# Kernel optimization log

Hardware: AMD Instinct MI355X
Metric: run time of the kernel (lower is better)

The kernel has to match this reference:

```python
import jax, jax.numpy as jnp
import numpy as np

DIM = 1024
HEADS = 16
HEAD_DIM = DIM // HEADS
FF = 4096
B, S = 2, 2048
EPS = 1e-6
NEG = float(jnp.finfo(jnp.float32).min)


def rmsnorm(x, w):
    return x * jax.lax.rsqrt(jnp.mean(x * x, axis=-1, keepdims=True) + EPS) * w


def setup_inputs() -> dict:
    key = jax.random.key(0)
    ks = jax.random.split(key, 12)
    s = 1.0 / np.sqrt(DIM)
    return {
        "x": jax.random.normal(ks[0], (B, S, DIM), jnp.float32),
        "src_key_padding_mask": jax.random.randint(ks[1], (B, S), 0, 2).astype(bool),
        "rel_pos_bias": jax.random.normal(ks[2], (1, HEADS, S, S), jnp.float32),
        "Wq": jax.random.normal(ks[3], (DIM, DIM), jnp.float32) * s,
        "Wk": jax.random.normal(ks[4], (DIM, DIM), jnp.float32) * s,
        "Wv": jax.random.normal(ks[5], (DIM, DIM), jnp.float32) * s,
        "Wo": jax.random.normal(ks[6], (DIM, DIM), jnp.float32) * s,
        "W1": jax.random.normal(ks[7], (DIM, FF), jnp.float32) * s,
        "b1": jnp.zeros((FF,), jnp.float32),
        "W2": jax.random.normal(ks[8], (FF, DIM), jnp.float32) * (1.0 / np.sqrt(FF)),
        "b2": jnp.zeros((DIM,), jnp.float32),
        "g1": jnp.ones((DIM,), jnp.float32),
        "g2": jnp.ones((DIM,), jnp.float32),
    }


def reference(x, src_key_padding_mask, rel_pos_bias, Wq, Wk, Wv, Wo, W1, b1, W2, b2, g1, g2):
    # pre-norm self-attention
    h = rmsnorm(x, g1)  # [B,S,D]
    q = (h @ Wq).reshape(B, S, HEADS, HEAD_DIM).transpose(0, 2, 1, 3)
    k = (h @ Wk).reshape(B, S, HEADS, HEAD_DIM).transpose(0, 2, 1, 3)
    v = (h @ Wv).reshape(B, S, HEADS, HEAD_DIM).transpose(0, 2, 1, 3)
    scale = HEAD_DIM ** -0.5
    scores = jnp.einsum('bhqd,bhkd->bhqk', q, k) * scale + rel_pos_bias
    scores = jnp.where(src_key_padding_mask[:, None, None, :], NEG, scores)
    attn = jax.nn.softmax(scores, axis=-1)
    out = jnp.einsum('bhqk,bhkd->bhqd', attn, v)
    out = out.transpose(0, 2, 1, 3).reshape(B, S, DIM) @ Wo
    x = x + out
    # GELU FFN (exact erf gelu, matching torch F.gelu default)
    h2 = rmsnorm(x, g2)
    h2 = jax.nn.gelu(h2 @ W1 + b1, approximate=False) @ W2 + b2
    return x + h2
```

## Files before the change

kernel.cpp:

```cpp
#include <hip/hip_runtime.h>
#include <math.h>

typedef __attribute__((ext_vector_type(8))) short   short8;
typedef __attribute__((ext_vector_type(4))) short   short4v;
typedef __attribute__((ext_vector_type(8))) __bf16  bf16x8;
typedef __attribute__((ext_vector_type(4))) float   f32x4;
typedef __attribute__((ext_vector_type(16))) float  f32x16;
typedef unsigned short u16;

#define DIMD 1024
#define NHEAD 16
#define HD 64
#define FFD 4096
#define BB 2
#define SSEQ 2048
#define NSPLIT 2
#define KVSPAN (SSEQ / NSPLIT)
#define NROWS (BB * NHEAD * SSEQ)
#define NEGF -3.4028235e38f

__device__ __forceinline__ u16 f2bf(float f){
  unsigned u = __float_as_uint(f);
  u += 0x7FFFu + ((u >> 16) & 1u);
  return (u16)(u >> 16);
}
__device__ __forceinline__ float bf2f(u16 v){
  return __uint_as_float(((unsigned)v) << 16);
}
__device__ __forceinline__ void gload16(const u16* g, u16* l){
  __builtin_amdgcn_global_load_lds((const __attribute__((address_space(1))) void*)g,
                                   (__attribute__((address_space(3))) void*)l, 16, 0, 0);
}

__global__ void normalize_mask(const unsigned char* __restrict__ m, unsigned char* __restrict__ outm){
  __shared__ int any;
  if (threadIdx.x == 0) any = 0;
  __syncthreads();
  int bad = 0;
  for (int i = threadIdx.x; i < BB * SSEQ; i += 1024)
    if ((i & 3) && m[i]) bad = 1;
  if (bad) atomicOr(&any, 1);
  __syncthreads();
  bool is_i32 = (any == 0);
  if (is_i32){
    const int* mi = (const int*)m;
    for (int k = threadIdx.x; k < BB * SSEQ; k += 1024)
      outm[k] = (unsigned char)(mi[k] != 0);
  } else {
    for (int k = threadIdx.x; k < BB * SSEQ; k += 1024)
      outm[k] = m[k] ? 1 : 0;
  }
}

__global__ void transpose_to_bf16(const float* __restrict__ W, u16* __restrict__ Wt, int K, int N){
  __shared__ float tile[32][33];
  int n0 = blockIdx.x * 32, k0 = blockIdx.y * 32;
  int tx = threadIdx.x, ty = threadIdx.y;
  #pragma unroll
  for (int i = 0; i < 32; i += 8)
    tile[ty + i][tx] = W[(size_t)(k0 + ty + i) * N + n0 + tx];
  __syncthreads();
  #pragma unroll
  for (int i = 0; i < 32; i += 8)
    Wt[(size_t)(n0 + ty + i) * K + k0 + tx] = f2bf(tile[tx][ty + i]);
}

__global__ void vtrans(const u16* __restrict__ qkv, u16* __restrict__ vt){
  __shared__ u16 tile[32][33];
  int s0 = blockIdx.x * 32, d0 = blockIdx.y * 32;
  int bh = blockIdx.z;
  int b = bh >> 4, h = bh & 15;
  int tx = threadIdx.x, ty = threadIdx.y;
  const u16* src = qkv + (size_t)(b * SSEQ) * 3072 + 2048 + h * HD + d0;
  #pragma unroll
  for (int i = 0; i < 32; i += 8)
    tile[ty + i][tx] = src[(size_t)(s0 + ty + i) * 3072 + tx];
  __syncthreads();
  u16* dst = vt + ((size_t)bh * HD + d0) * SSEQ + s0;
  #pragma unroll
  for (int i = 0; i < 32; i += 8)
    dst[(size_t)(ty + i) * SSEQ + tx] = tile[tx][ty + i];
}

__global__ __launch_bounds__(256) void rmsnorm_k(const float* __restrict__ x, const float* __restrict__ g,
                                                 u16* __restrict__ out, int D){
  int row = blockIdx.x;
  const float* xr = x + (size_t)row * D;
  float ss = 0.f;
  for (int i = threadIdx.x * 4; i < D; i += 1024){
    float4 v = *(const float4*)&xr[i];
    ss += v.x*v.x + v.y*v.y + v.z*v.z + v.w*v.w;
  }
  #pragma unroll
  for (int o = 32; o > 0; o >>= 1) ss += __shfl_down(ss, o);
  __shared__ float red[4];
  if ((threadIdx.x & 63) == 0) red[threadIdx.x >> 6] = ss;
  __syncthreads();
  float tot = red[0] + red[1] + red[2] + red[3];
  float rs = rsqrtf(tot / (float)D + 1e-6f);
  for (int i = threadIdx.x * 4; i < D; i += 1024){
    float4 v  = *(const float4*)&xr[i];
    float4 gv = *(const float4*)&g[i];
    ushort4 o4;
    o4.x = f2bf(v.x * rs * gv.x);
    o4.y = f2bf(v.y * rs * gv.y);
    o4.z = f2bf(v.z * rs * gv.z);
    o4.w = f2bf(v.w * rs * gv.w);
    *(ushort4*)&out[(size_t)row * D + i] = o4;
  }
}

__device__ __forceinline__ void xcd_swz(int& bx, int& by){
  int gx = gridDim.x, nwg = gx * gridDim.y;
  int flat = by * gx + bx;
  int q = nwg >> 3;
  flat = (flat & 7) * q + (flat >> 3);
  bx = flat % gx;
  by = flat / gx;
}

template<int EPI>
__global__ __launch_bounds__(512, 2) void gemm8p(const u16* __restrict__ A, const u16* __restrict__ Bt,
                                                 u16* __restrict__ outb, const float* __restrict__ bias,
                                                 int M, int N, int K){
  extern __shared__ u16 lds[];
  const int tid = threadIdx.x;
  const int lane = tid & 63, lr = lane >> 4, lc = lane & 15;
  const int wid = tid >> 6, wr = wid >> 2, wc = wid & 3;
  int bx = blockIdx.x, by = blockIdx.y;
  xcd_swz(bx, by);
  const int m0 = by * 256, n0 = bx * 256;
  const int NT = K >> 5;
  const int slot8 = ((lr ^ (lc & 3)) << 3);

  f32x4 acc[8][4];
  #pragma unroll
  for (int i = 0; i < 8; i++)
    #pragma unroll
    for (int j = 0; j < 4; j++) acc[i][j] = (f32x4){0.f,0.f,0.f,0.f};

  const int srow = tid >> 2;
  const int scg  = (tid & 3) ^ (srow & 3);

  auto stage = [&](int t, int buf, int rsel){
    int row = ((rsel & 1) << 7) + srow;
    const u16* src = ((rsel < 2) ? A + (size_t)(m0 + row) * K
                                 : Bt + (size_t)(n0 + row) * K) + t * 32 + scg * 8;
    u16* dst = lds + buf * 16384 + ((rsel & 2) << 12) + ((rsel & 1) << 12) + tid * 8;
    gload16(src, dst);
  };
  auto ldA = [&](int buf, int mi) -> bf16x8 {
    int ra = wr * 128 + mi * 16 + lc;
    return *(const bf16x8*)&lds[buf * 16384 + ra * 32 + slot8];
  };
  auto ldB = [&](int buf, int ni) -> bf16x8 {
    int rb = wc * 64 + ni * 16 + lc;
    return *(const bf16x8*)&lds[buf * 16384 + 8192 + rb * 32 + slot8];
  };

  #pragma unroll
  for (int rs = 0; rs < 4; rs++) stage(0, 0, rs);
  #pragma unroll
  for (int rs = 0; rs < 4; rs++) stage(1, 1, rs);
  asm volatile("s_waitcnt vmcnt(4)" ::: "memory");
  __builtin_amdgcn_s_barrier();

  int buf = 0;
  for (int t = 0; t < NT; t++){
    int sbuf = buf + 2; if (sbuf >= 3) sbuf -= 3;
    bool ds = (t + 2 < NT);
    bf16x8 a[4], b[4];
    #pragma unroll
    for (int mi = 0; mi < 4; mi++) a[mi] = ldA(buf, mi);
    #pragma unroll
    for (int ni = 0; ni < 4; ni++) b[ni] = ldB(buf, ni);
    if (ds){ stage(t + 2, sbuf, 0); stage(t + 2, sbuf, 1); }
    __builtin_amdgcn_s_barrier();
    __builtin_amdgcn_s_setprio(1);
    #pragma unroll
    for (int mi = 0; mi < 4; mi++)
      #pragma unroll
      for (int ni = 0; ni < 4; ni++)
        acc[mi][ni] = __builtin_amdgcn_mfma_f32_16x16x32_bf16(a[mi], b[ni], acc[mi][ni], 0, 0, 0);
    __builtin_amdgcn_s_setprio(0);
    __builtin_amdgcn_s_barrier();
    #pragma unroll
    for (int mi = 0; mi < 4; mi++) a[mi] = ldA(buf, mi + 4);
    if (ds){ stage(t + 2, sbuf, 2); stage(t + 2, sbuf, 3); }
    __builtin_amdgcn_s_barrier();
    __builtin_amdgcn_s_setprio(1);
    #pragma unroll
    for (int mi = 0; mi < 4; mi++)
      #pragma unroll
      for (int ni = 0; ni < 4; ni++)
        acc[mi + 4][ni] = __builtin_amdgcn_mfma_f32_16x16x32_bf16(a[mi], b[ni], acc[mi + 4][ni], 0, 0, 0);
    __builtin_amdgcn_s_setprio(0);
    if (t + 2 < NT)      { asm volatile("s_waitcnt vmcnt(4)" ::: "memory"); }
    else if (t + 1 < NT) { asm volatile("s_waitcnt vmcnt(0)" ::: "memory"); }
    __builtin_amdgcn_s_barrier();
    buf++; if (buf == 3) buf = 0;
  }

  #pragma unroll
  for (int mi = 0; mi < 8; mi++){
    #pragma unroll
    for (int ni = 0; ni < 4; ni++){
      int col = n0 + wc * 64 + ni * 16 + lc;
      #pragma unroll
      for (int r = 0; r < 4; r++){
        int row = m0 + wr * 128 + mi * 16 + lr * 4 + r;
        float v = acc[mi][ni][r];
        if (EPI == 2){
          v += bias[col];
          v = 0.5f * v * (1.f + erff(v * 0.70710678118654752f));
        }
        outb[(size_t)row * N + col] = f2bf(v);
      }
    }
  }
}

template<int EPI, int BN>
__global__ __launch_bounds__(256) void gemm_bt(const u16* __restrict__ A, const u16* __restrict__ Bt,
                                               u16* __restrict__ outb, float* __restrict__ outf,
                                               const float* __restrict__ bias, const float* __restrict__ resid,
                                               int M, int N, int K){
  constexpr int NI = BN / 32;
  __shared__ u16 As[128 * 64];
  __shared__ u16 Bs[BN * 64];
  const int tid = threadIdx.x;
  const int wid = tid >> 6, lane = tid & 63, lr = lane >> 4, lc = lane & 15;
  const int wr = wid >> 1, wc = wid & 1;
  int bx = blockIdx.x, by = blockIdx.y;
  xcd_swz(bx, by);
  const int m0 = by * 128, n0 = bx * BN;

  f32x4 acc[4][NI];
  #pragma unroll
  for (int i = 0; i < 4; i++)
    #pragma unroll
    for (int j = 0; j < NI; j++) acc[i][j] = (f32x4){0.f,0.f,0.f,0.f};

  for (int k0 = 0; k0 < K; k0 += 64){
    __syncthreads();
    #pragma unroll
    for (int j = 0; j < 4; j++){
      int c = tid + 256 * j;
      gload16(A + (size_t)(m0 + (c >> 3)) * K + k0 + (c & 7) * 8, As + c * 8);
    }
    #pragma unroll
    for (int j = 0; j < NI; j++){
      int c = tid + 256 * j;
      gload16(Bt + (size_t)(n0 + (c >> 3)) * K + k0 + (c & 7) * 8, Bs + c * 8);
    }
    __syncthreads();
    #pragma unroll
    for (int kk = 0; kk < 2; kk++){
      bf16x8 a[4], b[NI];
      #pragma unroll
      for (int mi = 0; mi < 4; mi++) a[mi] = *(const bf16x8*)&As[(wr*64 + mi*16 + lc)*64 + kk*32 + lr*8];
      #pragma unroll
      for (int ni = 0; ni < NI; ni++) b[ni] = *(const bf16x8*)&Bs[(wc*(BN/2) + ni*16 + lc)*64 + kk*32 + lr*8];
      #pragma unroll
      for (int mi = 0; mi < 4; mi++)
        #pragma unroll
        for (int ni = 0; ni < NI; ni++)
          acc[mi][ni] = __builtin_amdgcn_mfma_f32_16x16x32_bf16(a[mi], b[ni], acc[mi][ni], 0, 0, 0);
    }
  }

  #pragma unroll
  for (int mi = 0; mi < 4; mi++){
    #pragma unroll
    for (int ni = 0; ni < NI; ni++){
      #pragma unroll
      for (int r = 0; r < 4; r++){
        int row = m0 + wr*64 + mi*16 + lr*4 + r;
        int col = n0 + wc*(BN/2) + ni*16 + lc;
        float v = acc[mi][ni][r];
        size_t idx = (size_t)row * N + col;
        if (EPI == 0){
          outb[idx] = f2bf(v);
        } else if (EPI == 1){
          outf[idx] = v + resid[idx];
        } else if (EPI == 2){
          v += bias[col];
          v = 0.5f * v * (1.f + erff(v * 0.70710678118654752f));
          outb[idx] = f2bf(v);
        } else {
          outf[idx] = v + bias[col] + resid[idx];
        }
      }
    }
  }
}

__global__ __launch_bounds__(256) void attn_part(const u16* __restrict__ qkv, const u16* __restrict__ vt,
                                                 const float* __restrict__ bias,
                                                 const unsigned char* __restrict__ mask,
                                                 u16* __restrict__ Opart, float* __restrict__ mp, float* __restrict__ lp){
  __shared__ u16 Ks [64 * 64];
  __shared__ u16 Vts[64 * 64];
  __shared__ u16 Ps [4 * 32 * 72];

  const int tid = threadIdx.x;
  const int lane = tid & 63, hi = lane >> 5, lq = lane & 31;
  const int wq = tid >> 6;
  const int b  = blockIdx.x & 1;
  const int qb = blockIdx.x >> 1;
  const int h  = blockIdx.y;
  const int sp = blockIdx.z;
  const int qw = qb * 128 + wq * 32;
  const int kv_lo = sp * KVSPAN, kv_hi = kv_lo + KVSPAN;

  char* kls = (char*)Ks;
  char* vls = (char*)Vts;
  u16*  psw = Ps + wq * 32 * 72;

  bf16x8 qf[4];
  {
    const u16* qp = qkv + ((size_t)(b * SSEQ + qw + lq)) * 3072 + h * HD + hi * 8;
    #pragma unroll
    for (int dstep = 0; dstep < 4; dstep++) qf[dstep] = *(const bf16x8*)(qp + dstep * 16);
  }

  const u16* kbase = qkv + (size_t)b * SSEQ * 3072 + 1024 + h * HD;
  const u16* vbase = vt + (size_t)(b * NHEAD + h) * HD * SSEQ;
  const int c0 = tid, c1 = tid + 256;
  auto kaddr = [&](int kv0, int c){ return kbase + (size_t)(kv0 + (c >> 3)) * 3072 + (c & 7) * 8; };
  auto vaddr = [&](int kv0, int c){ return vbase + (size_t)(c >> 3) * SSEQ + kv0 + (c & 7) * 8; };
  auto sstore = [&](char* base, int c, short8 v){
    int byte = (c >> 3) * 128 + (c & 7) * 16;
    byte ^= ((c >> 3) & 7) << 4;
    *(short8*)(base + byte) = v;
  };

  const float* brow = bias + ((size_t)h * SSEQ + (qw + lq)) * SSEQ;
  const unsigned char* mbase = mask + b * SSEQ;

  short8 kr0 = *(const short8*)kaddr(kv_lo, c0);
  short8 kr1 = *(const short8*)kaddr(kv_lo, c1);
  short8 vr0 = *(const short8*)vaddr(kv_lo, c0);
  short8 vr1 = *(const short8*)vaddr(kv_lo, c1);

  float mrow = NEGF, lsum = 0.f;
  f32x16 oacc[2];
  #pragma unroll
  for (int g = 0; g < 2; g++)
    #pragma unroll
    for (int r = 0; r < 16; r++) oacc[g][r] = 0.f;

  for (int kv0 = kv_lo; kv0 < kv_hi; kv0 += 64){
    float4 bv[8]; unsigned mk[8];
    #pragma unroll
    for (int kg = 0; kg < 2; kg++)
      #pragma unroll
      for (int rq = 0; rq < 4; rq++){
        int base = kv0 + kg * 32 + 8 * rq + 4 * hi;
        bv[kg*4+rq] = *(const float4*)&brow[base];
        mk[kg*4+rq] = *(const unsigned*)&mbase[base];
      }

    __syncthreads();
    sstore(kls, c0, kr0); sstore(kls, c1, kr1);
    sstore(vls, c0, vr0); sstore(vls, c1, vr1);
    __syncthreads();

    {
      int nxt = (kv0 + 64 < kv_hi) ? kv0 + 64 : kv_lo;
      kr0 = *(const short8*)kaddr(nxt, c0);
      kr1 = *(const short8*)kaddr(nxt, c1);
      vr0 = *(const short8*)vaddr(nxt, c0);
      vr1 = *(const short8*)vaddr(nxt, c1);
    }

    f32x16 acc[2];
    #pragma unroll
    for (int g = 0; g < 2; g++)
      #pragma unroll
      for (int r = 0; r < 16; r++) acc[g][r] = 0.f;
    __builtin_amdgcn_s_setprio(1);
    #pragma unroll
    for (int kg = 0; kg < 2; kg++){
      int row = kg * 32 + lq;
      #pragma unroll
      for (int dstep = 0; dstep < 4; dstep++){
        int byte = row * 128 + dstep * 32 + hi * 16;
        byte ^= (row & 7) << 4;
        bf16x8 kf = *(const bf16x8*)(kls + byte);
        acc[kg] = __builtin_amdgcn_mfma_f32_32x32x16_bf16(kf, qf[dstep], acc[kg], 0, 0, 0);
      }
    }
    __builtin_amdgcn_s_setprio(0);

    float p[2][16];
    float tm = NEGF;
    #pragma unroll
    for (int kg = 0; kg < 2; kg++)
      #pragma unroll
      for (int r = 0; r < 16; r++){
        int g = kg * 4 + (r >> 2);
        bool m = ((mk[g] >> (8 * (r & 3))) & 0xffu) != 0;
        float v = acc[kg][r] * 0.125f + ((const float*)&bv[g])[r & 3];
        v = m ? NEGF : v;
        p[kg][r] = v;
        tm = fmaxf(tm, v);
      }
    tm = fmaxf(tm, __shfl_xor(tm, 32));

    if (__any(tm > mrow + 5.f)){
      float mnew = fmaxf(mrow, tm);
      float corr = __expf(mrow - mnew);
      lsum *= corr;
      mrow = mnew;
      #pragma unroll
      for (int r = 0; r < 16; r++){
        float cr = __shfl(corr, (r & 3) + 8 * (r >> 2) + 4 * hi);
        oacc[0][r] *= cr;
        oacc[1][r] *= cr;
      }
    }

    float psum = 0.f;
    #pragma unroll
    for (int kg = 0; kg < 2; kg++)
      #pragma unroll
      for (int r = 0; r < 16; r++){
        float sv = p[kg][r];
        float e = (sv < -1e30f) ? 0.f : __expf(sv - mrow);
        p[kg][r] = e;
        psum += e;
      }
    psum += __shfl_xor(psum, 32);
    lsum += psum;

    #pragma unroll
    for (int kg = 0; kg < 2; kg++)
      #pragma unroll
      for (int rq = 0; rq < 4; rq++){
        short4v pk;
        #pragma unroll
        for (int t = 0; t < 4; t++)
          pk[t] = (short)(__float_as_uint(p[kg][rq * 4 + t]) >> 16);
        *(short4v*)&psw[lq * 72 + kg * 32 + 8 * rq + 4 * hi] = pk;
      }

    __builtin_amdgcn_s_setprio(1);
    #pragma unroll
    for (int ks = 0; ks < 4; ks++){
      bf16x8 pa = *(const bf16x8*)&psw[lq * 72 + ks * 16 + hi * 8];
      #pragma unroll
      for (int dgrp = 0; dgrp < 2; dgrp++){
        int row = dgrp * 32 + lq;
        int byte = row * 128 + ks * 32 + hi * 16;
        byte ^= (row & 7) << 4;
        bf16x8 vf = *(const bf16x8*)(vls + byte);
        oacc[dgrp] = __builtin_amdgcn_mfma_f32_32x32x16_bf16(pa, vf, oacc[dgrp], 0, 0, 0);
      }
    }
    __builtin_amdgcn_s_setprio(0);
  }

  if (lane < 32){
    int ridx = (b * NHEAD + h) * SSEQ + qw + lq;
    mp[sp * NROWS + ridx] = mrow;
    lp[sp * NROWS + ridx] = lsum;
  }
  #pragma unroll
  for (int r = 0; r < 16; r++){
    int qloc = (r & 3) + 8 * (r >> 2) + 4 * hi;
    int ridx = (b * NHEAD + h) * SSEQ + qw + qloc;
    size_t o = ((size_t)(sp * NROWS + ridx)) * HD;
    Opart[o + lq]      = f2bf(oacc[0][r]);
    Opart[o + 32 + lq] = f2bf(oacc[1][r]);
  }
}

__global__ __launch_bounds__(256) void attn_merge(const u16* __restrict__ Opart, const float* __restrict__ mp,
                                                  const float* __restrict__ lp, u16* __restrict__ attn){
  int row = blockIdx.x * 16 + (threadIdx.x >> 4);
  int tx = threadIdx.x & 15;
  float ms[NSPLIT], ls[NSPLIT];
  float m = NEGF;
  #pragma unroll
  for (int sp = 0; sp < NSPLIT; sp++){
    ms[sp] = mp[sp * NROWS + row];
    ls[sp] = lp[sp * NROWS + row];
    if (ls[sp] > 0.f) m = fmaxf(m, ms[sp]);
  }
  float acc0 = 0.f, acc1 = 0.f, acc2 = 0.f, acc3 = 0.f, ltot = 0.f;
  #pragma unroll
  for (int sp = 0; sp < NSPLIT; sp++){
    float e = (ls[sp] > 0.f) ? __expf(ms[sp] - m) : 0.f;
    ltot += ls[sp] * e;
    ushort4 o4 = *(const ushort4*)&Opart[((size_t)(sp * NROWS + row)) * HD + tx*4];
    acc0 += e * bf2f(o4.x);
    acc1 += e * bf2f(o4.y);
    acc2 += e * bf2f(o4.z);
    acc3 += e * bf2f(o4.w);
  }
  float inv = ltot > 0.f ? 1.f / ltot : 0.f;
  int b = row >> 15, h = (row >> 11) & 15, q = row & 2047;
  ushort4 r4;
  r4.x = f2bf(acc0 * inv);
  r4.y = f2bf(acc1 * inv);
  r4.z = f2bf(acc2 * inv);
  r4.w = f2bf(acc3 * inv);
  *(ushort4*)&attn[((size_t)(b * SSEQ + q)) * DIMD + h * HD + tx*4] = r4;
}

extern "C" void kernel_launch(void* const* d_in, const int* in_sizes, int n_in,
                              void* d_out, int out_size, void* d_ws, size_t ws_size,
                              hipStream_t stream){
  const float* x    = (const float*)d_in[0];
  const unsigned char* mask = (const unsigned char*)d_in[1];
  const float* bias = (const float*)d_in[2];
  const float* Wq   = (const float*)d_in[3];
  const float* Wk   = (const float*)d_in[4];
  const float* Wv   = (const float*)d_in[5];
  const float* Wo   = (const float*)d_in[6];
  const float* W1   = (const float*)d_in[7];
  const float* b1   = (const float*)d_in[8];
  const float* W2   = (const float*)d_in[9];
  const float* b2   = (const float*)d_in[10];
  const float* g1   = (const float*)d_in[11];
  const float* g2   = (const float*)d_in[12];
  float* out = (float*)d_out;

  char* ws = (char*)d_ws;
  size_t off = 0;
  auto take = [&](size_t bytes) -> char* {
    char* p = ws + off;
    off = (off + bytes + 255) & ~(size_t)255;
    return p;
  };
  u16*  wqkv_t = (u16*) take((size_t)3072*1024*2);
  u16*  wo_t   = (u16*) take((size_t)1024*1024*2);
  u16*  w1_t   = (u16*) take((size_t)4096*1024*2);
  u16*  w2_t   = (u16*) take((size_t)1024*4096*2);
  u16*  hbuf   = (u16*) take((size_t)4096*1024*2);
  u16*  qkv    = (u16*) take((size_t)4096*3072*2);
  u16*  attn   = (u16*) take((size_t)4096*1024*2);
  float* x2    = (float*)take((size_t)4096*1024*4);
  u16*  h2     = (u16*) take((size_t)4096*1024*2);
  u16*  fbuf   = (u16*) take((size_t)4096*4096*2);
  unsigned char* nmask = (unsigned char*)take(BB*SSEQ);
  float* mpbuf = (float*)take((size_t)NSPLIT*NROWS*4);
  float* lpbuf = (float*)take((size_t)NSPLIT*NROWS*4);
  u16* Opart = fbuf;
  u16* vt_g  = hbuf;

  hipFuncSetAttribute(reinterpret_cast<const void*>(gemm8p<0>),
                      hipFuncAttributeMaxDynamicSharedMemorySize, 98304);
  hipFuncSetAttribute(reinterpret_cast<const void*>(gemm8p<2>),
                      hipFuncAttributeMaxDynamicSharedMemorySize, 98304);

  normalize_mask<<<1, 1024, 0, stream>>>(mask, nmask);

  dim3 tb(32, 8);
  transpose_to_bf16<<<dim3(32, 32),  tb, 0, stream>>>(Wq, wqkv_t,                      1024, 1024);
  transpose_to_bf16<<<dim3(32, 32),  tb, 0, stream>>>(Wk, wqkv_t + (size_t)1024*1024,  1024, 1024);
  transpose_to_bf16<<<dim3(32, 32),  tb, 0, stream>>>(Wv, wqkv_t + (size_t)2048*1024,  1024, 1024);
  transpose_to_bf16<<<dim3(32, 32),  tb, 0, stream>>>(Wo, wo_t,                        1024, 1024);
  transpose_to_bf16<<<dim3(128, 32), tb, 0, stream>>>(W1, w1_t,                        1024, 4096);
  transpose_to_bf16<<<dim3(32, 128), tb, 0, stream>>>(W2, w2_t,                        4096, 1024);

  rmsnorm_k<<<4096, 256, 0, stream>>>(x, g1, hbuf, DIMD);

  gemm8p<0><<<dim3(3072/256, 4096/256), 512, 98304, stream>>>(hbuf, wqkv_t, qkv, nullptr, 4096, 3072, 1024);

  vtrans<<<dim3(SSEQ/32, 2, BB*NHEAD), tb, 0, stream>>>(qkv, vt_g);

  attn_part<<<dim3(2*SSEQ/128, NHEAD, NSPLIT), 256, 0, stream>>>(qkv, vt_g, bias, nmask, Opart, mpbuf, lpbuf);
  attn_merge<<<dim3(NROWS/16), 256, 0, stream>>>(Opart, mpbuf, lpbuf, attn);

  gemm_bt<1,64><<<dim3(1024/64, 4096/128), 256, 0, stream>>>(attn, wo_t, nullptr, x2, nullptr, x, 4096, 1024, 1024);

  rmsnorm_k<<<4096, 256, 0, stream>>>(x2, g2, h2, DIMD);

  gemm8p<2><<<dim3(4096/256, 4096/256), 512, 98304, stream>>>(h2, w1_t, fbuf, b1, 4096, 4096, 1024);

  gemm_bt<3,64><<<dim3(1024/64, 4096/128), 256, 0, stream>>>(fbuf, w2_t, nullptr, out, b2, x2, 4096, 1024, 4096);
}
```

Before: 376.0 us.

## Split-K FFN2 GEMM with 256x256 tiles and merge kernel; batch QKVO weight transposes

The FFN down-projection moves from a 128x64-tile GEMM to a 256x256-tile pipelined MFMA kernel split four ways along K. Each split writes a bf16 partial, and a separate merge kernel sums the partials and adds the bias and residual. This is meant to raise MFMA efficiency and occupancy for the N=1024 output. The four 1024x1024 weight transposes are also merged into one launch. The cost is the extra partial-buffer traffic, plus precision loss from rounding the partials to bf16 before summing.

```diff
diff --git a/kernel.cpp b/kernel.cpp
--- a/kernel.cpp
+++ b/kernel.cpp
@@ -65,6 +65,29 @@
     Wt[(size_t)(n0 + ty + i) * K + k0 + tx] = f2bf(tile[tx][ty + i]);
 }
 
+__global__ void transpose4_to_bf16(const float* __restrict__ Wq, const float* __restrict__ Wk,
+                                   const float* __restrict__ Wv, const float* __restrict__ Wo,
+                                   u16* __restrict__ Tqkv, u16* __restrict__ To){
+  __shared__ float tile[32][33];
+  const float* W;
+  u16* T;
+  switch (blockIdx.z){
+    case 0: W = Wq; T = Tqkv;                        break;
+    case 1: W = Wk; T = Tqkv + (size_t)1024*1024;    break;
+    case 2: W = Wv; T = Tqkv + (size_t)2048*1024;    break;
+    default: W = Wo; T = To;                         break;
+  }
+  int n0 = blockIdx.x * 32, k0 = blockIdx.y * 32;
+  int tx = threadIdx.x, ty = threadIdx.y;
+  #pragma unroll
+  for (int i = 0; i < 32; i += 8)
+    tile[ty + i][tx] = W[(size_t)(k0 + ty + i) * 1024 + n0 + tx];
+  __syncthreads();
+  #pragma unroll
+  for (int i = 0; i < 32; i += 8)
+    T[(size_t)(n0 + ty + i) * 1024 + k0 + tx] = f2bf(tile[tx][ty + i]);
+}
+
 __global__ void vtrans(const u16* __restrict__ qkv, u16* __restrict__ vt){
   __shared__ u16 tile[32][33];
   int s0 = blockIdx.x * 32, d0 = blockIdx.y * 32;
@@ -218,6 +241,127 @@
       }
     }
   }
+}
+
+__global__ __launch_bounds__(512, 2) void gemm8p_sk(const u16* __restrict__ A, const u16* __restrict__ Bt,
+                                                    u16* __restrict__ part,
+                                                    int M, int N, int Kstride, int Klen){
+  extern __shared__ u16 lds[];
+  const int tid = threadIdx.x;
+  const int lane = tid & 63, lr = lane >> 4, lc = lane & 15;
+  const int wid = tid >> 6, wr = wid >> 2, wc = wid & 3;
+  int bx = blockIdx.x, by = blockIdx.y;
+  xcd_swz(bx, by);
+  const int sk = blockIdx.z;
+  const size_t koff = (size_t)sk * Klen;
+  const int m0 = by * 256, n0 = bx * 256;
+  const int NT = Klen >> 5;
+  const int slot8 = ((lr ^ (lc & 3)) << 3);
+
+  f32x4 acc[8][4];
+  #pragma unroll
+  for (int i = 0; i < 8; i++)
+    #pragma unroll
+    for (int j = 0; j < 4; j++) acc[i][j] = (f32x4){0.f,0.f,0.f,0.f};
+
+  const int srow = tid >> 2;
+  const int scg  = (tid & 3) ^ (srow & 3);
+
+  auto stage = [&](int t, int buf, int rsel){
+    int row = ((rsel & 1) << 7) + srow;
+    const u16* src = ((rsel < 2) ? A + (size_t)(m0 + row) * Kstride
+                                 : Bt + (size_t)(n0 + row) * Kstride) + koff + t * 32 + scg * 8;
+    u16* dst = lds + buf * 16384 + ((rsel & 2) << 12) + ((rsel & 1) << 12) + tid * 8;
+    gload16(src, dst);
+  };
+  auto ldA = [&](int buf, int mi) -> bf16x8 {
+    int ra = wr * 128 + mi * 16 + lc;
+    return *(const bf16x8*)&lds[buf * 16384 + ra * 32 + slot8];
+  };
+  auto ldB = [&](int buf, int ni) -> bf16x8 {
+    int rb = wc * 64 + ni * 16 + lc;
+    return *(const bf16x8*)&lds[buf * 16384 + 8192 + rb * 32 + slot8];
+  };
+
+  #pragma unroll
+  for (int rs = 0; rs < 4; rs++) stage(0, 0, rs);
+  #pragma unroll
+  for (int rs = 0; rs < 4; rs++) stage(1, 1, rs);
+  asm volatile("s_waitcnt vmcnt(4)" ::: "memory");
+  __builtin_amdgcn_s_barrier();
+
+  int buf = 0;
+  for (int t = 0; t < NT; t++){
+    int sbuf = buf + 2; if (sbuf >= 3) sbuf -= 3;
+    bool ds = (t + 2 < NT);
+    bf16x8 a[4], b[4];
+    #pragma unroll
+    for (int mi = 0; mi < 4; mi++) a[mi] = ldA(buf, mi);
+    #pragma unroll
+    for (int ni = 0; ni < 4; ni++) b[ni] = ldB(buf, ni);
+    if (ds){ stage(t + 2, sbuf, 0); stage(t + 2, sbuf, 1); }
+    __builtin_amdgcn_s_barrier();
+    __builtin_amdgcn_s_setprio(1);
+    #pragma unroll
+    for (int mi = 0; mi < 4; mi++)
+      #pragma unroll
+      for (int ni = 0; ni < 4; ni++)
+        acc[mi][ni] = __builtin_amdgcn_mfma_f32_16x16x32_bf16(a[mi], b[ni], acc[mi][ni], 0, 0, 0);
+    __builtin_amdgcn_s_setprio(0);
+    __builtin_amdgcn_s_barrier();
+    #pragma unroll
+    for (int mi = 0; mi < 4; mi++) a[mi] = ldA(buf, mi + 4);
+    if (ds){ stage(t + 2, sbuf, 2); stage(t + 2, sbuf, 3); }
+    __builtin_amdgcn_s_barrier();
+    __builtin_amdgcn_s_setprio(1);
+    #pragma unroll
+    for (int mi = 0; mi < 4; mi++)
+      #pragma unroll
+      for (int ni = 0; ni < 4; ni++)
+        acc[mi + 4][ni] = __builtin_amdgcn_mfma_f32_16x16x32_bf16(a[mi], b[ni], acc[mi + 4][ni], 0, 0, 0);
+    __builtin_amdgcn_s_setprio(0);
+    if (t + 2 < NT)      { asm volatile("s_waitcnt vmcnt(4)" ::: "memory"); }
+    else if (t + 1 < NT) { asm volatile("s_waitcnt vmcnt(0)" ::: "memory"); }
+    __builtin_amdgcn_s_barrier();
+    buf++; if (buf == 3) buf = 0;
+  }
+
+  u16* po = part + (size_t)sk * M * N;
+  #pragma unroll
+  for (int mi = 0; mi < 8; mi++){
+    #pragma unroll
+    for (int ni = 0; ni < 4; ni++){
+      int col = n0 + wc * 64 + ni * 16 + lc;
+      #pragma unroll
+      for (int r = 0; r < 4; r++){
+        int row = m0 + wr * 128 + mi * 16 + lr * 4 + r;
+        po[(size_t)row * N + col] = f2bf(acc[mi][ni][r]);
+      }
+    }
+  }
+}
+
+__global__ __launch_bounds__(256) void ffn2_merge(const u16* __restrict__ part, const float* __restrict__ x2,
+                                                  const float* __restrict__ b2, float* __restrict__ out){
+  size_t i = ((size_t)blockIdx.x * 256 + threadIdx.x) * 8;
+  int col = (int)(i & (DIMD - 1));
+  const size_t MN = (size_t)4096 * DIMD;
+  short8 a0 = *(const short8*)&part[i];
+  short8 a1 = *(const short8*)&part[MN + i];
+  short8 a2 = *(const short8*)&part[2 * MN + i];
+  short8 a3 = *(const short8*)&part[3 * MN + i];
+  float r[8];
+  #pragma unroll
+  for (int j = 0; j < 8; j++)
+    r[j] = (bf2f((u16)a0[j]) + bf2f((u16)a1[j])) + (bf2f((u16)a2[j]) + bf2f((u16)a3[j]));
+  float4 xa = *(const float4*)&x2[i];
+  float4 xb = *(const float4*)&x2[i + 4];
+  float4 ba = *(const float4*)&b2[col];
+  float4 bb = *(const float4*)&b2[col + 4];
+  float4 o0 = {r[0] + xa.x + ba.x, r[1] + xa.y + ba.y, r[2] + xa.z + ba.z, r[3] + xa.w + ba.w};
+  float4 o1 = {r[4] + xb.x + bb.x, r[5] + xb.y + bb.y, r[6] + xb.z + bb.z, r[7] + xb.w + bb.w};
+  *(float4*)&out[i] = o0;
+  *(float4*)&out[i + 4] = o1;
 }
 
 template<int EPI, int BN>
@@ -547,6 +691,7 @@
   unsigned char* nmask = (unsigned char*)take(BB*SSEQ);
   float* mpbuf = (float*)take((size_t)NSPLIT*NROWS*4);
   float* lpbuf = (float*)take((size_t)NSPLIT*NROWS*4);
+  u16*  fp2    = (u16*) take((size_t)4*4096*1024*2);
   u16* Opart = fbuf;
   u16* vt_g  = hbuf;
 
@@ -554,16 +699,15 @@
                       hipFuncAttributeMaxDynamicSharedMemorySize, 98304);
   hipFuncSetAttribute(reinterpret_cast<const void*>(gemm8p<2>),
                       hipFuncAttributeMaxDynamicSharedMemorySize, 98304);
+  hipFuncSetAttribute(reinterpret_cast<const void*>(gemm8p_sk),
+                      hipFuncAttributeMaxDynamicSharedMemorySize, 98304);
 
   normalize_mask<<<1, 1024, 0, stream>>>(mask, nmask);
 
   dim3 tb(32, 8);
-  transpose_to_bf16<<<dim3(32, 32),  tb, 0, stream>>>(Wq, wqkv_t,                      1024, 1024);
-  transpose_to_bf16<<<dim3(32, 32),  tb, 0, stream>>>(Wk, wqkv_t + (size_t)1024*1024,  1024, 1024);
-  transpose_to_bf16<<<dim3(32, 32),  tb, 0, stream>>>(Wv, wqkv_t + (size_t)2048*1024,  1024, 1024);
-  transpose_to_bf16<<<dim3(32, 32),  tb, 0, stream>>>(Wo, wo_t,                        1024, 1024);
-  transpose_to_bf16<<<dim3(128, 32), tb, 0, stream>>>(W1, w1_t,                        1024, 4096);
-  transpose_to_bf16<<<dim3(32, 128), tb, 0, stream>>>(W2, w2_t,                        4096, 1024);
+  transpose4_to_bf16<<<dim3(32, 32, 4), tb, 0, stream>>>(Wq, Wk, Wv, Wo, wqkv_t, wo_t);
+  transpose_to_bf16<<<dim3(128, 32), tb, 0, stream>>>(W1, w1_t, 1024, 4096);
+  transpose_to_bf16<<<dim3(32, 128), tb, 0, stream>>>(W2, w2_t, 4096, 1024);
 
   rmsnorm_k<<<4096, 256, 0, stream>>>(x, g1, hbuf, DIMD);
 
@@ -580,5 +724,6 @@
 
   gemm8p<2><<<dim3(4096/256, 4096/256), 512, 98304, stream>>>(h2, w1_t, fbuf, b1, 4096, 4096, 1024);
 
-  gemm_bt<3,64><<<dim3(1024/64, 4096/128), 256, 0, stream>>>(fbuf, w2_t, nullptr, out, b2, x2, 4096, 1024, 4096);
-}
+  gemm8p_sk<<<dim3(1024/256, 4096/256, 4), 512, 98304, stream>>>(fbuf, w2_t, fp2, 4096, 1024, 4096, 1024);
+  ffn2_merge<<<dim3(4096*1024/2048), 256, 0, stream>>>(fp2, x2, b2, out);
+}
```

Result: faster. 335.1 us (-10.9%).
